# Optimization experiments

Measured on AMD Instinct MI355X. Metric: run time of the kernel, lower is better.

The kernel has to match this reference:

```python
import jax, jax.numpy as jnp
import numpy as np

T, B, I, H = 1200, 32, 512, 512


def setup_inputs() -> dict:
    key = jax.random.key(0)
    ks = jax.random.split(key, 10)
    s = 0.1
    x = jax.random.normal(ks[0], (T, B, I), dtype=jnp.float32)
    lengths = jax.random.randint(ks[1], (B,), 1, T + 1)
    lengths = lengths.at[0].set(T)  # ensure padded output length == T (static shape)
    return {
        "x": x,
        "output_lengths": lengths,
        "w_ih_fwd": jax.random.normal(ks[2], (4 * H, I), dtype=jnp.float32) * s,
        "w_hh_fwd": jax.random.normal(ks[3], (4 * H, H), dtype=jnp.float32) * s,
        "b_ih_fwd": jax.random.normal(ks[4], (4 * H,), dtype=jnp.float32) * s,
        "b_hh_fwd": jax.random.normal(ks[5], (4 * H,), dtype=jnp.float32) * s,
        "w_ih_bwd": jax.random.normal(ks[6], (4 * H, I), dtype=jnp.float32) * s,
        "w_hh_bwd": jax.random.normal(ks[7], (4 * H, H), dtype=jnp.float32) * s,
        "b_ih_bwd": jax.random.normal(ks[8], (4 * H,), dtype=jnp.float32) * s,
        "b_hh_bwd": jax.random.normal(ks[9], (4 * H,), dtype=jnp.float32) * s,
    }


def _lstm_dir(x, mask, w_ih, w_hh, b_ih, b_hh):
    """Masked unidirectional LSTM (PyTorch gate order i,f,g,o).
    x: (T,B,I), mask: (T,B,1) bool. Returns outputs (T,B,H), (h_n, c_n)."""
    h0 = jnp.zeros((x.shape[1], w_hh.shape[1]), dtype=x.dtype)
    c0 = jnp.zeros_like(h0)
    # Precompute input projection for all timesteps at once (one big GEMM).
    x_proj = jnp.einsum('tbi,gi->tbg', x, w_ih) + (b_ih + b_hh)

    def step(carry, inp):
        h, c = carry
        xp, m = inp  # xp: (B,4H), m: (B,1)
        gates = xp + h @ w_hh.T
        i, f, g, o = jnp.split(gates, 4, axis=-1)
        i = jax.nn.sigmoid(i)
        f = jax.nn.sigmoid(f)
        g = jnp.tanh(g)
        o = jax.nn.sigmoid(o)
        c_new = f * c + i * g
        h_new = o * jnp.tanh(c_new)
        # Packed semantics: state frozen past each sequence's length.
        h = jnp.where(m, h_new, h)
        c = jnp.where(m, c_new, c)
        out = jnp.where(m, h_new, jnp.zeros_like(h_new))  # pad positions -> 0
        return (h, c), out

    (h_n, c_n), outs = jax.lax.scan(step, (h0, c0), (x_proj, mask))
    return outs, h_n, c_n


def reference(x, output_lengths, w_ih_fwd, w_hh_fwd, b_ih_fwd, b_hh_fwd,
              w_ih_bwd, w_hh_bwd, b_ih_bwd, b_hh_bwd):
    t_idx = jnp.arange(x.shape[0])  # (T,)
    mask = (t_idx[:, None] < output_lengths[None, :])[:, :, None]  # (T,B,1)

    # Forward direction.
    out_f, h_f, c_f = _lstm_dir(x, mask, w_ih_fwd, w_hh_fwd, b_ih_fwd, b_hh_fwd)

    # Backward direction: reverse each sequence within its valid region.
    rev_idx = jnp.clip(output_lengths[None, :] - 1 - t_idx[:, None], 0)  # (T,B)
    x_rev = jnp.take_along_axis(x, rev_idx[:, :, None], axis=0) * mask
    out_r, h_b, c_b = _lstm_dir(x_rev, mask, w_ih_bwd, w_hh_bwd, b_ih_bwd, b_hh_bwd)
    out_b = jnp.take_along_axis(out_r, rev_idx[:, :, None], axis=0) * mask

    # Bidirectional view(...,2,-1).sum(2) == sum of direction outputs.
    out = out_f + out_b
    h_n = jnp.stack([h_f, h_b], axis=0)  # (2,B,H)
    c_n = jnp.stack([c_f, c_b], axis=0)
    return out, h_n, c_n
```

## Files before the change

kernel.cpp:

```cpp
#include <hip/hip_runtime.h>
#include <cstdint>
#include <cstddef>

typedef unsigned short u16;
typedef unsigned long long u64;
typedef short bf16x8 __attribute__((ext_vector_type(8)));
typedef float f32x4 __attribute__((ext_vector_type(4)));
typedef unsigned short u16x4 __attribute__((ext_vector_type(4)));

#define T_LEN 1200

#define O_X     0ull
#define O_WIH   39321600ull
#define O_WHH   43515904ull
#define O_BIAS  47710208ull
#define O_HBUF  47726592ull
#define O_FLG   47857664ull
#define WS_NEED 47861760ull

#define HO 19660800ull
#define CO 19693568ull

#define HROW 516

__device__ __forceinline__ u16 f2bf(float f) {
  union { float f; unsigned u; } v; v.f = f;
  unsigned r = v.u + 0x7FFFu + ((v.u >> 16) & 1u);
  return (u16)(r >> 16);
}
__device__ __forceinline__ float sigm(float x) { return 1.f / (1.f + __expf(-x)); }
__device__ __forceinline__ float tanh_s(float x) {
  float ax = fabsf(x);
  float e = __expf(-2.f * ax);
  float t = (1.f - e) / (1.f + e);
  return x < 0.f ? -t : t;
}

__device__ __forceinline__ u64 ld_dev64(const u16* p) {
  return __hip_atomic_load((const u64*)p, __ATOMIC_RELAXED, __HIP_MEMORY_SCOPE_AGENT);
}
__device__ __forceinline__ void st_dev32(u16* p, unsigned v) {
  __hip_atomic_store((unsigned*)p, v, __ATOMIC_RELAXED, __HIP_MEMORY_SCOPE_AGENT);
}

__global__ __launch_bounds__(256) void cast_x_k(const float4* __restrict__ x,
                                                u16* __restrict__ xb) {
  int i = blockIdx.x * 256 + threadIdx.x;
  float4 v = x[i];
  u16x4 o;
  o.x = f2bf(v.x); o.y = f2bf(v.y); o.z = f2bf(v.z); o.w = f2bf(v.w);
  *(u16x4*)(xb + (size_t)i * 4) = o;
}

__global__ __launch_bounds__(256) void prep_w_k(
    const float* __restrict__ wih_f, const float* __restrict__ whh_f,
    const float* __restrict__ bih_f, const float* __restrict__ bhh_f,
    const float* __restrict__ wih_b, const float* __restrict__ whh_b,
    const float* __restrict__ bih_b, const float* __restrict__ bhh_b,
    u16* __restrict__ Wih, u16* __restrict__ Whh, float* __restrict__ bias) {
  int tid = blockIdx.x * 256 + threadIdx.x;
  int g = tid >> 9;
  float vi, vh;
  if (g < 2048) { vi = wih_f[tid]; vh = whh_f[tid]; }
  else { int t2 = tid - (2048 * 512); vi = wih_b[t2]; vh = whh_b[t2]; }
  Wih[tid] = f2bf(vi);
  Whh[tid] = f2bf(vh);
  if ((tid & 511) == 0) {
    bias[g] = (g < 2048) ? (bih_f[g] + bhh_f[g]) : (bih_b[g - 2048] + bhh_b[g - 2048]);
  }
}

__global__ __launch_bounds__(256, 1) void lstm_rec(const u16* __restrict__ X,
                                                   const u16* __restrict__ Wih,
                                                   const u16* __restrict__ Whh,
                                                   const float* __restrict__ bias,
                                                   const int* __restrict__ lengths,
                                                   u16* __restrict__ hbuf,
                                                   float* __restrict__ out,
                                                   unsigned* __restrict__ flags) {
  const int tid = threadIdx.x, lane = tid & 63, wid = tid >> 6;
  const int bx = blockIdx.x;
  const int dir = bx >> 5, slice = bx & 31, c0 = slice * 16;
  const int quad = lane >> 4, l15 = lane & 15;

  __shared__ alignas(16) u16 h_l[32 * HROW];
  __shared__ float h_m[32][16];
  __shared__ float c_m[32][16];
  __shared__ float pre[4][32][16];
  __shared__ int len_s[32];

  if (tid < 32) len_s[tid] = lengths[tid];
  h_m[tid >> 4][tid & 15] = 0.f;          c_m[tid >> 4][tid & 15] = 0.f;
  h_m[(tid + 256) >> 4][tid & 15] = 0.f;  c_m[(tid + 256) >> 4][tid & 15] = 0.f;

  bf16x8 bh[16], bxw[16];
  {
    const size_t wrow = (size_t)(dir * 2048 + wid * 512 + c0 + l15) * 512 + quad * 8;
#pragma unroll
    for (int ks = 0; ks < 16; ++ks) {
      bh[ks]  = *(const bf16x8*)(Whh + wrow + (size_t)ks * 32);
      bxw[ks] = *(const bf16x8*)(Wih + wrow + (size_t)ks * 32);
    }
  }
  __syncthreads();

  const int b0 = tid >> 4, colv = tid & 15, b1 = b0 + 16;
  const int hcol = c0 + colv;
  const float bi  = bias[dir * 2048 + 0 * 512 + hcol];
  const float bfv = bias[dir * 2048 + 1 * 512 + hcol];
  const float bg  = bias[dir * 2048 + 2 * 512 + hcol];
  const float bo  = bias[dir * 2048 + 3 * 512 + hcol];

  unsigned* myflag = flags + (size_t)bx * 16;
  const unsigned* pollflag = flags + (size_t)(dir * 32 + (lane & 31)) * 16;

  for (int t = 0; t < T_LEN; ++t) {
    const u16* hb = hbuf + (size_t)((t & 1) * 32768 + dir * 16384);
    u16* hbw      = hbuf + (size_t)(((t + 1) & 1) * 32768 + dir * 16384);

    const int ba = l15, bb = 16 + l15;
    int lena = len_s[ba], lenb = len_s[bb];
    int tta = (dir == 0) ? t : (lena - 1 - t);  if (tta < 0) tta = 0;
    int ttb = (dir == 0) ? t : (lenb - 1 - t);  if (ttb < 0) ttb = 0;
    const u16* xrow0 = X + ((size_t)tta * 32 + ba) * 512 + quad * 8;
    const u16* xrow1 = X + ((size_t)ttb * 32 + bb) * 512 + quad * 8;
    bf16x8 ax0[16], ax1[16];
#pragma unroll
    for (int ks = 0; ks < 16; ++ks) {
      ax0[ks] = *(const bf16x8*)(xrow0 + (size_t)ks * 32);
      ax1[ks] = *(const bf16x8*)(xrow1 + (size_t)ks * 32);
    }

    if (wid == 0) {
      for (;;) {
        unsigned v = __hip_atomic_load(pollflag, __ATOMIC_RELAXED, __HIP_MEMORY_SCOPE_AGENT);
        if (__all((int)(v >= (unsigned)t))) break;
        __builtin_amdgcn_s_sleep(1);
      }
    }
    __syncthreads();
    asm volatile("" ::: "memory");

    u64 hstg[16];
#pragma unroll
    for (int j = 0; j < 16; ++j)
      hstg[j] = ld_dev64(hb + j * 1024 + tid * 4);

    f32x4 a0x = {0.f,0.f,0.f,0.f}, a1x = {0.f,0.f,0.f,0.f};
#pragma unroll
    for (int ks = 0; ks < 16; ++ks) {
      a0x = __builtin_amdgcn_mfma_f32_16x16x32_bf16(ax0[ks], bxw[ks], a0x, 0, 0, 0);
      a1x = __builtin_amdgcn_mfma_f32_16x16x32_bf16(ax1[ks], bxw[ks], a1x, 0, 0, 0);
    }

#pragma unroll
    for (int j = 0; j < 16; ++j) {
      int g = j * 1024 + tid * 4;
      *(u64*)&h_l[(g >> 9) * HROW + (g & 511)] = hstg[j];
    }
    __syncthreads();

    f32x4 a0h = {0.f,0.f,0.f,0.f}, a1h = {0.f,0.f,0.f,0.f};
    const u16* hl0 = h_l + (size_t)l15 * HROW + quad * 8;
    const u16* hl1 = h_l + (size_t)(16 + l15) * HROW + quad * 8;
#pragma unroll
    for (int ks = 0; ks < 16; ++ks) {
      bf16x8 f0 = *(const bf16x8*)(hl0 + ks * 32);
      bf16x8 f1 = *(const bf16x8*)(hl1 + ks * 32);
      a0h = __builtin_amdgcn_mfma_f32_16x16x32_bf16(f0, bh[ks], a0h, 0, 0, 0);
      a1h = __builtin_amdgcn_mfma_f32_16x16x32_bf16(f1, bh[ks], a1h, 0, 0, 0);
    }
    f32x4 acc0 = a0x + a0h, acc1 = a1x + a1h;
#pragma unroll
    for (int r = 0; r < 4; ++r) {
      pre[wid][quad * 4 + r][l15]      = acc0[r];
      pre[wid][16 + quad * 4 + r][l15] = acc1[r];
    }
    __syncthreads();

    int len0 = len_s[b0], len1 = len_s[b1];
    int tt0 = (dir == 0) ? t : (len0 - 1 - t);
    int tt1 = (dir == 0) ? t : (len1 - 1 - t);
    bool m0 = (dir == 0) ? (t < len0) : (tt0 >= 0);
    bool m1 = (dir == 0) ? (t < len1) : (tt1 >= 0);
    if (tt0 < 0) tt0 = 0;
    if (tt1 < 0) tt1 = 0;

    float hold0 = h_m[b0][colv], hold1 = h_m[b1][colv];
    float hn0 = 0.f, hn1 = 0.f;
    if (m0) {
      float gi = pre[0][b0][colv] + bi,  gf = pre[1][b0][colv] + bfv;
      float gg = pre[2][b0][colv] + bg,  go = pre[3][b0][colv] + bo;
      float cn = sigm(gf) * c_m[b0][colv] + sigm(gi) * tanh_s(gg);
      hn0 = sigm(go) * tanh_s(cn);
      c_m[b0][colv] = cn; h_m[b0][colv] = hn0; hold0 = hn0;
    }
    if (m1) {
      float gi = pre[0][b1][colv] + bi,  gf = pre[1][b1][colv] + bfv;
      float gg = pre[2][b1][colv] + bg,  go = pre[3][b1][colv] + bo;
      float cn = sigm(gf) * c_m[b1][colv] + sigm(gi) * tanh_s(gg);
      hn1 = sigm(go) * tanh_s(cn);
      c_m[b1][colv] = cn; h_m[b1][colv] = hn1; hold1 = hn1;
    }

    unsigned p0 = (unsigned)f2bf(hold0), p1 = (unsigned)f2bf(hold1);
    unsigned q0 = (unsigned)__shfl_xor((int)p0, 1);
    unsigned q1 = (unsigned)__shfl_xor((int)p1, 1);
    if ((colv & 1) == 0) {
      st_dev32(hbw + (size_t)b0 * 512 + hcol, p0 | (q0 << 16));
      st_dev32(hbw + (size_t)b1 * 512 + hcol, p1 | (q1 << 16));
    }
    asm volatile("" ::: "memory");
    __syncthreads();
    if (tid == 0)
      __hip_atomic_store(myflag, (unsigned)(t + 1), __ATOMIC_RELAXED, __HIP_MEMORY_SCOPE_AGENT);

    if (m0) atomicAdd(out + (size_t)(tt0 * 32 + b0) * 512 + hcol, hn0);
    if (m1) atomicAdd(out + (size_t)(tt1 * 32 + b1) * 512 + hcol, hn1);
  }

  out[HO + (size_t)dir * 16384 + (size_t)b0 * 512 + hcol] = h_m[b0][colv];
  out[HO + (size_t)dir * 16384 + (size_t)b1 * 512 + hcol] = h_m[b1][colv];
  out[CO + (size_t)dir * 16384 + (size_t)b0 * 512 + hcol] = c_m[b0][colv];
  out[CO + (size_t)dir * 16384 + (size_t)b1 * 512 + hcol] = c_m[b1][colv];
}

extern "C" void kernel_launch(void* const* d_in, const int* in_sizes, int n_in,
                              void* d_out, int out_size, void* d_ws, size_t ws_size,
                              hipStream_t stream) {
  const float* x     = (const float*)d_in[0];
  const int*   lens  = (const int*)d_in[1];
  const float* wih_f = (const float*)d_in[2];
  const float* whh_f = (const float*)d_in[3];
  const float* bih_f = (const float*)d_in[4];
  const float* bhh_f = (const float*)d_in[5];
  const float* wih_b = (const float*)d_in[6];
  const float* whh_b = (const float*)d_in[7];
  const float* bih_b = (const float*)d_in[8];
  const float* bhh_b = (const float*)d_in[9];
  float* out = (float*)d_out;
  char* ws = (char*)d_ws;

  u16*      xb   = (u16*)(ws + O_X);
  u16*      Wih  = (u16*)(ws + O_WIH);
  u16*      Whh  = (u16*)(ws + O_WHH);
  float*    bias = (float*)(ws + O_BIAS);
  u16*      hbuf = (u16*)(ws + O_HBUF);
  unsigned* flg  = (unsigned*)(ws + O_FLG);

  hipMemsetAsync(hbuf, 0, 131072 + 4096, stream);
  hipMemsetAsync(d_out, 0, (size_t)out_size * 4, stream);

  cast_x_k<<<19200, 256, 0, stream>>>((const float4*)x, xb);
  prep_w_k<<<8192, 256, 0, stream>>>(wih_f, whh_f, bih_f, bhh_f,
                                     wih_b, whh_b, bih_b, bhh_b, Wih, Whh, bias);
  lstm_rec<<<64, 256, 0, stream>>>(xb, Wih, Whh, bias, lens, hbuf, out, flg);
}
```

Measured before the change: 10.98 ms.

## Replace per-block flag barrier with step-tagged hidden-state words polled directly

Drops the separate per-block progress flags and the extra barrier/flag store. Each hidden value is now written as a 32-bit word holding the bf16 value and the step number, and consumers spin on the data itself until every tag matches the current step. Cell and hidden state move from shared memory into registers, and the input and recurrent MFMA accumulators are merged. This removes one barrier and a flag round trip per step, but doubles the hidden-state traffic per step and makes the poll loop re-read all 32 staged words on any mismatch.

```diff
diff --git a/kernel.cpp b/kernel.cpp
--- a/kernel.cpp
+++ b/kernel.cpp
@@ -3,6 +3,7 @@
 #include <cstddef>
 
 typedef unsigned short u16;
+typedef unsigned int u32;
 typedef unsigned long long u64;
 typedef short bf16x8 __attribute__((ext_vector_type(8)));
 typedef float f32x4 __attribute__((ext_vector_type(4)));
@@ -15,8 +16,7 @@
 #define O_WHH   43515904ull
 #define O_BIAS  47710208ull
 #define O_HBUF  47726592ull
-#define O_FLG   47857664ull
-#define WS_NEED 47861760ull
+#define WS_NEED 47988736ull
 
 #define HO 19660800ull
 #define CO 19693568ull
@@ -36,11 +36,11 @@
   return x < 0.f ? -t : t;
 }
 
-__device__ __forceinline__ u64 ld_dev64(const u16* p) {
+__device__ __forceinline__ u64 ld_dev64(const u32* p) {
   return __hip_atomic_load((const u64*)p, __ATOMIC_RELAXED, __HIP_MEMORY_SCOPE_AGENT);
 }
-__device__ __forceinline__ void st_dev32(u16* p, unsigned v) {
-  __hip_atomic_store((unsigned*)p, v, __ATOMIC_RELAXED, __HIP_MEMORY_SCOPE_AGENT);
+__device__ __forceinline__ void st_dev32(u32* p, unsigned v) {
+  __hip_atomic_store(p, v, __ATOMIC_RELAXED, __HIP_MEMORY_SCOPE_AGENT);
 }
 
 __global__ __launch_bounds__(256) void cast_x_k(const float4* __restrict__ x,
@@ -75,23 +75,18 @@
                                                    const u16* __restrict__ Whh,
                                                    const float* __restrict__ bias,
                                                    const int* __restrict__ lengths,
-                                                   u16* __restrict__ hbuf,
-                                                   float* __restrict__ out,
-                                                   unsigned* __restrict__ flags) {
+                                                   u32* __restrict__ hbuf,
+                                                   float* __restrict__ out) {
   const int tid = threadIdx.x, lane = tid & 63, wid = tid >> 6;
   const int bx = blockIdx.x;
   const int dir = bx >> 5, slice = bx & 31, c0 = slice * 16;
   const int quad = lane >> 4, l15 = lane & 15;
 
   __shared__ alignas(16) u16 h_l[32 * HROW];
-  __shared__ float h_m[32][16];
-  __shared__ float c_m[32][16];
   __shared__ float pre[4][32][16];
   __shared__ int len_s[32];
 
   if (tid < 32) len_s[tid] = lengths[tid];
-  h_m[tid >> 4][tid & 15] = 0.f;          c_m[tid >> 4][tid & 15] = 0.f;
-  h_m[(tid + 256) >> 4][tid & 15] = 0.f;  c_m[(tid + 256) >> 4][tid & 15] = 0.f;
 
   bf16x8 bh[16], bxw[16];
   {
@@ -111,19 +106,18 @@
   const float bg  = bias[dir * 2048 + 2 * 512 + hcol];
   const float bo  = bias[dir * 2048 + 3 * 512 + hcol];
 
-  unsigned* myflag = flags + (size_t)bx * 16;
-  const unsigned* pollflag = flags + (size_t)(dir * 32 + (lane & 31)) * 16;
+  float hreg0 = 0.f, hreg1 = 0.f, creg0 = 0.f, creg1 = 0.f;
+  const int len0 = len_s[b0], len1 = len_s[b1];
+  const int lena = len_s[l15], lenb = len_s[16 + l15];
 
   for (int t = 0; t < T_LEN; ++t) {
-    const u16* hb = hbuf + (size_t)((t & 1) * 32768 + dir * 16384);
-    u16* hbw      = hbuf + (size_t)(((t + 1) & 1) * 32768 + dir * 16384);
-
-    const int ba = l15, bb = 16 + l15;
-    int lena = len_s[ba], lenb = len_s[bb];
+    u32* cur = hbuf + (size_t)(((t & 1) * 2 + dir) * 16384);
+    u32* nxt = hbuf + (size_t)((((t + 1) & 1) * 2 + dir) * 16384);
+
     int tta = (dir == 0) ? t : (lena - 1 - t);  if (tta < 0) tta = 0;
     int ttb = (dir == 0) ? t : (lenb - 1 - t);  if (ttb < 0) ttb = 0;
-    const u16* xrow0 = X + ((size_t)tta * 32 + ba) * 512 + quad * 8;
-    const u16* xrow1 = X + ((size_t)ttb * 32 + bb) * 512 + quad * 8;
+    const u16* xrow0 = X + ((size_t)tta * 32 + l15) * 512 + quad * 8;
+    const u16* xrow1 = X + ((size_t)ttb * 32 + 16 + l15) * 512 + quad * 8;
     bf16x8 ax0[16], ax1[16];
 #pragma unroll
     for (int ks = 0; ks < 16; ++ks) {
@@ -131,54 +125,52 @@
       ax1[ks] = *(const bf16x8*)(xrow1 + (size_t)ks * 32);
     }
 
-    if (wid == 0) {
-      for (;;) {
-        unsigned v = __hip_atomic_load(pollflag, __ATOMIC_RELAXED, __HIP_MEMORY_SCOPE_AGENT);
-        if (__all((int)(v >= (unsigned)t))) break;
-        __builtin_amdgcn_s_sleep(1);
-      }
+    u64 stg[32];
+#pragma unroll
+    for (int j = 0; j < 32; ++j)
+      stg[j] = ld_dev64(cur + j * 512 + tid * 2);
+
+    f32x4 a0 = {0.f,0.f,0.f,0.f}, a1 = {0.f,0.f,0.f,0.f};
+#pragma unroll
+    for (int ks = 0; ks < 16; ++ks) {
+      a0 = __builtin_amdgcn_mfma_f32_16x16x32_bf16(ax0[ks], bxw[ks], a0, 0, 0, 0);
+      a1 = __builtin_amdgcn_mfma_f32_16x16x32_bf16(ax1[ks], bxw[ks], a1, 0, 0, 0);
+    }
+
+    const u64 e2 = ((u64)(u32)t << 32) | (u32)t;
+    for (;;) {
+      u64 bad = 0;
+#pragma unroll
+      for (int j = 0; j < 32; ++j) bad |= (stg[j] ^ e2);
+      if ((bad & 0x0000FFFF0000FFFFull) == 0) break;
+#pragma unroll
+      for (int j = 0; j < 32; ++j)
+        stg[j] = ld_dev64(cur + j * 512 + tid * 2);
+    }
+
+#pragma unroll
+    for (int j = 0; j < 32; ++j) {
+      u32 d0 = (u32)stg[j], d1 = (u32)(stg[j] >> 32);
+      *(u32*)&h_l[j * HROW + tid * 2] = (d0 >> 16) | (d1 & 0xFFFF0000u);
     }
     __syncthreads();
-    asm volatile("" ::: "memory");
-
-    u64 hstg[16];
-#pragma unroll
-    for (int j = 0; j < 16; ++j)
-      hstg[j] = ld_dev64(hb + j * 1024 + tid * 4);
-
-    f32x4 a0x = {0.f,0.f,0.f,0.f}, a1x = {0.f,0.f,0.f,0.f};
-#pragma unroll
-    for (int ks = 0; ks < 16; ++ks) {
-      a0x = __builtin_amdgcn_mfma_f32_16x16x32_bf16(ax0[ks], bxw[ks], a0x, 0, 0, 0);
-      a1x = __builtin_amdgcn_mfma_f32_16x16x32_bf16(ax1[ks], bxw[ks], a1x, 0, 0, 0);
-    }
-
-#pragma unroll
-    for (int j = 0; j < 16; ++j) {
-      int g = j * 1024 + tid * 4;
-      *(u64*)&h_l[(g >> 9) * HROW + (g & 511)] = hstg[j];
-    }
-    __syncthreads();
-
-    f32x4 a0h = {0.f,0.f,0.f,0.f}, a1h = {0.f,0.f,0.f,0.f};
+
     const u16* hl0 = h_l + (size_t)l15 * HROW + quad * 8;
     const u16* hl1 = h_l + (size_t)(16 + l15) * HROW + quad * 8;
 #pragma unroll
     for (int ks = 0; ks < 16; ++ks) {
       bf16x8 f0 = *(const bf16x8*)(hl0 + ks * 32);
       bf16x8 f1 = *(const bf16x8*)(hl1 + ks * 32);
-      a0h = __builtin_amdgcn_mfma_f32_16x16x32_bf16(f0, bh[ks], a0h, 0, 0, 0);
-      a1h = __builtin_amdgcn_mfma_f32_16x16x32_bf16(f1, bh[ks], a1h, 0, 0, 0);
-    }
-    f32x4 acc0 = a0x + a0h, acc1 = a1x + a1h;
+      a0 = __builtin_amdgcn_mfma_f32_16x16x32_bf16(f0, bh[ks], a0, 0, 0, 0);
+      a1 = __builtin_amdgcn_mfma_f32_16x16x32_bf16(f1, bh[ks], a1, 0, 0, 0);
+    }
 #pragma unroll
     for (int r = 0; r < 4; ++r) {
-      pre[wid][quad * 4 + r][l15]      = acc0[r];
-      pre[wid][16 + quad * 4 + r][l15] = acc1[r];
+      pre[wid][quad * 4 + r][l15]      = a0[r];
+      pre[wid][16 + quad * 4 + r][l15] = a1[r];
     }
     __syncthreads();
 
-    int len0 = len_s[b0], len1 = len_s[b1];
     int tt0 = (dir == 0) ? t : (len0 - 1 - t);
     int tt1 = (dir == 0) ? t : (len1 - 1 - t);
     bool m0 = (dir == 0) ? (t < len0) : (tt0 >= 0);
@@ -186,43 +178,34 @@
     if (tt0 < 0) tt0 = 0;
     if (tt1 < 0) tt1 = 0;
 
-    float hold0 = h_m[b0][colv], hold1 = h_m[b1][colv];
     float hn0 = 0.f, hn1 = 0.f;
     if (m0) {
       float gi = pre[0][b0][colv] + bi,  gf = pre[1][b0][colv] + bfv;
       float gg = pre[2][b0][colv] + bg,  go = pre[3][b0][colv] + bo;
-      float cn = sigm(gf) * c_m[b0][colv] + sigm(gi) * tanh_s(gg);
+      float cn = sigm(gf) * creg0 + sigm(gi) * tanh_s(gg);
       hn0 = sigm(go) * tanh_s(cn);
-      c_m[b0][colv] = cn; h_m[b0][colv] = hn0; hold0 = hn0;
+      creg0 = cn; hreg0 = hn0;
     }
     if (m1) {
       float gi = pre[0][b1][colv] + bi,  gf = pre[1][b1][colv] + bfv;
       float gg = pre[2][b1][colv] + bg,  go = pre[3][b1][colv] + bo;
-      float cn = sigm(gf) * c_m[b1][colv] + sigm(gi) * tanh_s(gg);
+      float cn = sigm(gf) * creg1 + sigm(gi) * tanh_s(gg);
       hn1 = sigm(go) * tanh_s(cn);
-      c_m[b1][colv] = cn; h_m[b1][colv] = hn1; hold1 = hn1;
-    }
-
-    unsigned p0 = (unsigned)f2bf(hold0), p1 = (unsigned)f2bf(hold1);
-    unsigned q0 = (unsigned)__shfl_xor((int)p0, 1);
-    unsigned q1 = (unsigned)__shfl_xor((int)p1, 1);
-    if ((colv & 1) == 0) {
-      st_dev32(hbw + (size_t)b0 * 512 + hcol, p0 | (q0 << 16));
-      st_dev32(hbw + (size_t)b1 * 512 + hcol, p1 | (q1 << 16));
-    }
-    asm volatile("" ::: "memory");
-    __syncthreads();
-    if (tid == 0)
-      __hip_atomic_store(myflag, (unsigned)(t + 1), __ATOMIC_RELAXED, __HIP_MEMORY_SCOPE_AGENT);
+      creg1 = cn; hreg1 = hn1;
+    }
+
+    const u32 tag = (u32)(t + 1);
+    st_dev32(nxt + (size_t)b0 * 512 + hcol, ((u32)f2bf(hreg0) << 16) | tag);
+    st_dev32(nxt + (size_t)b1 * 512 + hcol, ((u32)f2bf(hreg1) << 16) | tag);
 
     if (m0) atomicAdd(out + (size_t)(tt0 * 32 + b0) * 512 + hcol, hn0);
     if (m1) atomicAdd(out + (size_t)(tt1 * 32 + b1) * 512 + hcol, hn1);
   }
 
-  out[HO + (size_t)dir * 16384 + (size_t)b0 * 512 + hcol] = h_m[b0][colv];
-  out[HO + (size_t)dir * 16384 + (size_t)b1 * 512 + hcol] = h_m[b1][colv];
-  out[CO + (size_t)dir * 16384 + (size_t)b0 * 512 + hcol] = c_m[b0][colv];
-  out[CO + (size_t)dir * 16384 + (size_t)b1 * 512 + hcol] = c_m[b1][colv];
+  out[HO + (size_t)dir * 16384 + (size_t)b0 * 512 + hcol] = hreg0;
+  out[HO + (size_t)dir * 16384 + (size_t)b1 * 512 + hcol] = hreg1;
+  out[CO + (size_t)dir * 16384 + (size_t)b0 * 512 + hcol] = creg0;
+  out[CO + (size_t)dir * 16384 + (size_t)b1 * 512 + hcol] = creg1;
 }
 
 extern "C" void kernel_launch(void* const* d_in, const int* in_sizes, int n_in,
@@ -241,18 +224,17 @@
   float* out = (float*)d_out;
   char* ws = (char*)d_ws;
 
-  u16*      xb   = (u16*)(ws + O_X);
-  u16*      Wih  = (u16*)(ws + O_WIH);
-  u16*      Whh  = (u16*)(ws + O_WHH);
-  float*    bias = (float*)(ws + O_BIAS);
-  u16*      hbuf = (u16*)(ws + O_HBUF);
-  unsigned* flg  = (unsigned*)(ws + O_FLG);
-
-  hipMemsetAsync(hbuf, 0, 131072 + 4096, stream);
+  u16*   xb   = (u16*)(ws + O_X);
+  u16*   Wih  = (u16*)(ws + O_WIH);
+  u16*   Whh  = (u16*)(ws + O_WHH);
+  float* bias = (float*)(ws + O_BIAS);
+  u32*   hbuf = (u32*)(ws + O_HBUF);
+
+  hipMemsetAsync(hbuf, 0, 262144, stream);
   hipMemsetAsync(d_out, 0, (size_t)out_size * 4, stream);
 
   cast_x_k<<<19200, 256, 0, stream>>>((const float4*)x, xb);
   prep_w_k<<<8192, 256, 0, stream>>>(wih_f, whh_f, bih_f, bhh_f,
                                      wih_b, whh_b, bih_b, bhh_b, Wih, Whh, bias);
-  lstm_rec<<<64, 256, 0, stream>>>(xb, Wih, Whh, bias, lens, hbuf, out, flg);
-}
+  lstm_rec<<<64, 256, 0, stream>>>(xb, Wih, Whh, bias, lens, hbuf, out);
+}
```

New measurement: 11.26 ms. 1.03x slower.
